# Optimization experiments

Hardware: AMD Instinct MI355X
Metric: run time of the kernel (lower is better)

Reference implementation:

```python
import jax, jax.numpy as jnp
import numpy as np

B, S, D, H, DFF = 2, 4096, 512, 8, 2048
DK = D // H
EPS = 1e-6


def layer_norm(x, alpha, bias):
    # torch: (x - mean) / (std + eps), std unbiased (ddof=1), eps added to std
    mean = jnp.mean(x, axis=-1, keepdims=True)
    std = jnp.std(x, axis=-1, keepdims=True, ddof=1)
    return alpha * (x - mean) / (std + EPS) + bias


def setup_inputs() -> dict:
    key = jax.random.key(0)
    ks = jax.random.split(key, 10)
    s = 0.02
    return {
        "x": jax.random.normal(ks[0], (B, S, D), jnp.float32),
        "mask": jax.random.randint(ks[1], (S, S), 0, 2, jnp.int32),
        "w_q": jax.random.normal(ks[2], (D, D), jnp.float32) * s,
        "w_k": jax.random.normal(ks[3], (D, D), jnp.float32) * s,
        "w_v": jax.random.normal(ks[4], (D, D), jnp.float32) * s,
        "w_o": jax.random.normal(ks[5], (D, D), jnp.float32) * s,
        "w1": jax.random.normal(ks[6], (D, DFF), jnp.float32) * s,
        "b1": jnp.zeros((DFF,), jnp.float32),
        "w2": jax.random.normal(ks[7], (DFF, D), jnp.float32) * s,
        "b2": jnp.zeros((D,), jnp.float32),
        "ln1_a": jnp.ones((D,), jnp.float32),
        "ln1_b": jnp.zeros((D,), jnp.float32),
        "ln2_a": jnp.ones((D,), jnp.float32),
        "ln2_b": jnp.zeros((D,), jnp.float32),
    }


def reference(x, mask, w_q, w_k, w_v, w_o, w1, b1, w2, b2, ln1_a, ln1_b, ln2_a, ln2_b):
    # --- sublayer 0: pre-norm self-attention with residual (dropout=0/eval) ---
    h = layer_norm(x, ln1_a, ln1_b)                       # [B,S,D]
    q = (h @ w_q).reshape(B, S, H, DK)
    k = (h @ w_k).reshape(B, S, H, DK)
    v = (h @ w_v).reshape(B, S, H, DK)
    scores = jnp.einsum("bqhd,bkhd->bhqk", q, k) / jnp.sqrt(jnp.float32(DK))
    scores = jnp.where(mask[None, None, :, :] == 0, jnp.float32(-1e9), scores)
    attn = jax.nn.softmax(scores, axis=-1)                # [B,H,S,S]
    ctx = jnp.einsum("bhqk,bkhd->bqhd", attn, v).reshape(B, S, D)
    x = x + ctx @ w_o
    # --- sublayer 1: pre-norm FFN with residual ---
    h2 = layer_norm(x, ln2_a, ln2_b)
    ff = jax.nn.relu(h2 @ w1 + b1) @ w2 + b2
    return x + ff
```

## Files before the change

### kernel.cpp

```cpp
#include <hip/hip_runtime.h>
#include <hip/hip_bf16.h>
#include <stdint.h>

#define S_LEN 4096
#define DMODEL 512
#define NHEAD 8
#define DHEAD 64
#define NTOK 8192

typedef unsigned short ushort_t;
typedef __attribute__((ext_vector_type(8))) short short8;
typedef __attribute__((ext_vector_type(4))) float f32x4;
typedef unsigned long long u64;
typedef __attribute__((ext_vector_type(2))) unsigned uint2v;

__device__ __forceinline__ float bf2f(ushort_t h) {
    union { unsigned u; float f; } c; c.u = ((unsigned)h) << 16; return c.f;
}
__device__ __forceinline__ ushort_t f2bf(float f) {
    union { float f; unsigned u; } c; c.f = f;
    unsigned u = c.u + 0x7fffu + ((c.u >> 16) & 1u);
    return (ushort_t)(u >> 16);
}
__device__ __forceinline__ void glds16(const ushort_t* g, ushort_t* l) {
    __builtin_amdgcn_global_load_lds(
        (const __attribute__((address_space(1))) unsigned int*)g,
        (__attribute__((address_space(3))) unsigned int*)l, 16, 0, 0);
}

__global__ __launch_bounds__(256) void maskbits_kernel(const int* __restrict__ mask,
        u64* __restrict__ mb) {
    size_t id = (size_t)blockIdx.x * 256 + threadIdx.x;
    int v = mask[id];
    u64 bits = __ballot(v != 0);
    if ((threadIdx.x & 63) == 0) mb[id >> 6] = bits;
}

__global__ __launch_bounds__(256) void masktrans_kernel(const u64* __restrict__ mb,
        u64* __restrict__ mbT) {
    int wid = (int)(((size_t)blockIdx.x * 256 + threadIdx.x) >> 6);
    int lane = threadIdx.x & 63;
    int gq = wid >> 7, kt = wid & 127;
    int lr = lane & 15, lg = lane >> 4;
    int row = gq * 16 + lr;
    u64* outp = mbT + ((size_t)gq * 128 + kt) * 8;
#pragma unroll
    for (int t = 0; t < 2; t++)
#pragma unroll
        for (int r = 0; r < 4; r++) {
            int col = kt * 32 + t * 16 + lg * 4 + r;
            u64 w = mb[(size_t)row * 64 + (col >> 6)];
            u64 bb = __ballot((unsigned)((w >> (col & 63)) & 1));
            if (lane == t * 4 + r) outp[t * 4 + r] = bb;
        }
}

__global__ __launch_bounds__(256) void wtrans_all(const float* __restrict__ wq,
        const float* __restrict__ wk, const float* __restrict__ wv,
        const float* __restrict__ wo, const float* __restrict__ w1,
        const float* __restrict__ w2,
        ushort_t* wqT, ushort_t* wkT, ushort_t* wvT, ushort_t* woT,
        ushort_t* w1T, ushort_t* w2T) {
    __shared__ __attribute__((aligned(16))) ushort_t t[64][72];
    int z = blockIdx.z;
    const float* src; ushort_t* dst; int R, C;
    switch (z) {
        case 0: src = wq; dst = wqT; R = 512;  C = 512;  break;
        case 1: src = wk; dst = wkT; R = 512;  C = 512;  break;
        case 2: src = wv; dst = wvT; R = 512;  C = 512;  break;
        case 3: src = wo; dst = woT; R = 512;  C = 512;  break;
        case 4: src = w1; dst = w1T; R = 512;  C = 2048; break;
        default: src = w2; dst = w2T; R = 2048; C = 512; break;
    }
    int r0 = blockIdx.x * 64, c0 = blockIdx.y * 64;
    if (r0 >= R || c0 >= C) return;
    int tid = threadIdx.x;
    for (int i = tid; i < 4096; i += 256) {
        int r = i >> 6, c = i & 63;
        t[r][c] = f2bf(src[(size_t)(r0 + r) * C + c0 + c]);
    }
    __syncthreads();
    for (int i = tid; i < 512; i += 256) {
        int c = i >> 3, rb = i & 7;
        short8 vv;
#pragma unroll
        for (int j = 0; j < 8; j++) ((ushort_t*)&vv)[j] = t[rb * 8 + j][c];
        *(short8*)(dst + (size_t)(c0 + c) * R + r0 + rb * 8) = vv;
    }
}

__global__ __launch_bounds__(256) void ln_f32(const float* __restrict__ x,
        const float* __restrict__ ga, const float* __restrict__ be,
        ushort_t* __restrict__ out) {
    int tok = blockIdx.x * 4 + (threadIdx.x >> 6);
    int lane = threadIdx.x & 63;
    const float* xr = x + (size_t)tok * DMODEL + lane * 8;
    f32x4 v0 = *(const f32x4*)xr;
    f32x4 v1 = *(const f32x4*)(xr + 4);
    float f[8];
    float s = 0.f, s2 = 0.f;
#pragma unroll
    for (int i = 0; i < 8; i++) {
        f[i] = (i < 4) ? v0[i] : v1[i - 4];
        s += f[i]; s2 += f[i] * f[i];
    }
#pragma unroll
    for (int off = 1; off < 64; off <<= 1) {
        s += __shfl_xor(s, off);
        s2 += __shfl_xor(s2, off);
    }
    float mean = s * (1.f / DMODEL);
    float var = (s2 - (float)DMODEL * mean * mean) * (1.f / (DMODEL - 1));
    var = fmaxf(var, 0.f);
    float inv = 1.f / (sqrtf(var) + 1e-6f);
    short8 o;
#pragma unroll
    for (int i = 0; i < 8; i++) {
        float val = ga[lane * 8 + i] * (f[i] - mean) * inv + be[lane * 8 + i];
        ((ushort_t*)&o)[i] = f2bf(val);
    }
    *(short8*)(out + (size_t)tok * DMODEL + lane * 8) = o;
}

__global__ __launch_bounds__(256) void out_init(const float* __restrict__ x2f,
        const float* __restrict__ b2, float* __restrict__ out) {
    size_t i = ((size_t)blockIdx.x * 256 + threadIdx.x) * 4;
    f32x4 v = *(const f32x4*)(x2f + i);
    f32x4 bb = *(const f32x4*)(b2 + (int)(i & 511));
    v = v + bb;
    *(f32x4*)(out + i) = v;
}

__global__ __launch_bounds__(256) void vtrans(const ushort_t* __restrict__ V,
        ushort_t* __restrict__ VT) {
    __shared__ __attribute__((aligned(16))) ushort_t t[64][72];
    int s0 = blockIdx.x * 64;
    int bh = blockIdx.y;
    int b = bh >> 3, h = bh & 7;
    int tid = threadIdx.x;
    const ushort_t* src = V + ((size_t)b * S_LEN + s0) * DMODEL + h * DHEAD;
    for (int i = tid; i < 512; i += 256) {
        int r = i >> 3, cb = i & 7;
        *(short8*)&t[r][cb * 8] = *(const short8*)(src + (size_t)r * DMODEL + cb * 8);
    }
    __syncthreads();
    ushort_t* dst = VT + (size_t)bh * DHEAD * S_LEN;
    for (int i = tid; i < 512; i += 256) {
        int d = i >> 3, rb = i & 7;
        short8 vv;
#pragma unroll
        for (int j = 0; j < 8; j++) ((ushort_t*)&vv)[j] = t[rb * 8 + j][d];
        *(short8*)(dst + (size_t)d * S_LEN + s0 + rb * 8) = vv;
    }
}

template <int MW, int NW>
__device__ __forceinline__ void gemm_body(const ushort_t* __restrict__ A,
        const ushort_t* __restrict__ BT, void* __restrict__ C,
        int N, int Klen, int kstride, int kbeg, float scale,
        const float* __restrict__ bias, const float* __restrict__ res,
        int relu, int cf32, int atomicc,
        ushort_t* As, ushort_t* Bs, int m0, int n0, int aoff, int coff) {
    int tid = threadIdx.x;
    int wave = tid >> 6, lane = tid & 63;
    int wm = wave >> 1, wn = wave & 1;
    int lr = lane & 15, lg = lane >> 4;
    int srow = lane >> 3, spos = lane & 7;
    int kst = (spos ^ srow) * 8;
    int rdk = lr & 7;
    f32x4 acc[MW][NW];
#pragma unroll
    for (int i = 0; i < MW; i++)
#pragma unroll
        for (int j = 0; j < NW; j++) acc[i][j] = (f32x4){0.f, 0.f, 0.f, 0.f};

    const ushort_t* Ag = A + (size_t)(m0 - aoff) * kstride + kbeg;
    const ushort_t* Bg = BT + (size_t)n0 * kstride + kbeg;

    for (int k0 = 0; k0 < Klen; k0 += 64) {
        __syncthreads();
        for (int ia = wave; ia < 4 * MW; ia += 4)
            glds16(Ag + (size_t)(ia * 8 + srow) * kstride + k0 + kst, As + ia * 8 * 64);
        for (int ib = wave; ib < 4 * NW; ib += 4)
            glds16(Bg + (size_t)(ib * 8 + srow) * kstride + k0 + kst, Bs + ib * 8 * 64);
        __syncthreads();
        short8 af[MW][2], bfv[NW][2];
#pragma unroll
        for (int t = 0; t < MW; t++) {
            const ushort_t* ar = As + (size_t)(wm * 16 * MW + t * 16 + lr) * 64;
            af[t][0] = *(const short8*)(ar + ((lg ^ rdk) * 8));
            af[t][1] = *(const short8*)(ar + (((lg + 4) ^ rdk) * 8));
        }
#pragma unroll
        for (int t = 0; t < NW; t++) {
            const ushort_t* br = Bs + (size_t)(wn * 16 * NW + t * 16 + lr) * 64;
            bfv[t][0] = *(const short8*)(br + ((lg ^ rdk) * 8));
            bfv[t][1] = *(const short8*)(br + (((lg + 4) ^ rdk) * 8));
        }
#pragma unroll
        for (int i = 0; i < MW; i++)
#pragma unroll
            for (int j = 0; j < NW; j++) {
                acc[i][j] = __builtin_amdgcn_mfma_f32_16x16x32_bf16(af[i][0], bfv[j][0], acc[i][j], 0, 0, 0);
                acc[i][j] = __builtin_amdgcn_mfma_f32_16x16x32_bf16(af[i][1], bfv[j][1], acc[i][j], 0, 0, 0);
            }
    }
#pragma unroll
    for (int i = 0; i < MW; i++) {
        int row = m0 + wm * 16 * MW + i * 16 + lg * 4;
#pragma unroll
        for (int j = 0; j < NW; j++) {
            int col = n0 + wn * 16 * NW + j * 16 + lr;
            float bb = bias ? bias[col] : 0.f;
#pragma unroll
            for (int r = 0; r < 4; r++) {
                float v = acc[i][j][r] * scale + bb;
                if (relu) v = fmaxf(v, 0.f);
                if (res) v += res[(size_t)(row + r) * N + col];
                size_t cidx = (size_t)(row + r - coff) * N + col;
                if (atomicc)   atomicAdd((float*)C + cidx, v);
                else if (cf32) ((float*)C)[cidx] = v;
                else           ((ushort_t*)C)[cidx] = f2bf(v);
            }
        }
    }
}

__global__ __launch_bounds__(256) void gemm_bt64(const ushort_t* __restrict__ A,
        const ushort_t* __restrict__ BT, void* __restrict__ C,
        int N, int K, float scale, const float* bias, const float* res, int relu,
        int cf32, int m_base, int aoff, int coff) {
    __shared__ __attribute__((aligned(16))) ushort_t As[64 * 64];
    __shared__ __attribute__((aligned(16))) ushort_t Bs[64 * 64];
    gemm_body<2, 2>(A, BT, C, N, K, K, 0, scale, bias, res, relu, cf32, 0, As, Bs,
                    m_base + blockIdx.x * 64, blockIdx.y * 64, aoff, coff);
}

__global__ __launch_bounds__(256) void gemm_w2sk(const ushort_t* __restrict__ A,
        const ushort_t* __restrict__ BT, float* __restrict__ C,
        int m_base, int aoff) {
    __shared__ __attribute__((aligned(16))) ushort_t As[64 * 64];
    __shared__ __attribute__((aligned(16))) ushort_t Bs[64 * 64];
    int kbeg = blockIdx.z * 1024;
    gemm_body<2, 2>(A, BT, C, 512, 1024, 2048, kbeg, 1.f, nullptr, nullptr, 0, 1, 1,
                    As, Bs, m_base + blockIdx.x * 64, blockIdx.y * 64, aoff, 0);
}

__global__ __launch_bounds__(256) void gemm_qkv(const ushort_t* __restrict__ A,
        const ushort_t* __restrict__ wqT, const ushort_t* __restrict__ wkT,
        const ushort_t* __restrict__ wvT,
        ushort_t* __restrict__ Q, ushort_t* __restrict__ Kb, ushort_t* __restrict__ V) {
    __shared__ __attribute__((aligned(16))) ushort_t As[128 * 64];
    __shared__ __attribute__((aligned(16))) ushort_t Bs[128 * 64];
    int z = blockIdx.z;
    const ushort_t* W = (z == 0) ? wqT : ((z == 1) ? wkT : wvT);
    ushort_t* O = (z == 0) ? Q : ((z == 1) ? Kb : V);
    float sc = (z == 0) ? 0.18033688011112042f : 1.f;
    gemm_body<4, 4>(A, W, O, DMODEL, DMODEL, DMODEL, 0, sc, nullptr, nullptr, 0, 0, 0,
                    As, Bs, blockIdx.x * 128, blockIdx.y * 128, 0, 0);
}

__global__ __launch_bounds__(128, 4) void attn_kernel(const ushort_t* __restrict__ Q,
        const ushort_t* __restrict__ K, const ushort_t* __restrict__ VT,
        const u64* __restrict__ mbT, ushort_t* __restrict__ Opart,
        float* __restrict__ lpart) {
    __shared__ __attribute__((aligned(16))) ushort_t Ks[2][32 * 64];
    __shared__ __attribute__((aligned(16))) ushort_t Vs[2][64 * 32];
    int qt = blockIdx.x, h = blockIdx.y, zz = blockIdx.z;
    int b = zz >> 1, half = zz & 1;
    int tid = threadIdx.x;
    int wv = __builtin_amdgcn_readfirstlane(tid >> 6);
    int lane = tid & 63;
    int lr = lane & 15, lg = lane >> 4;
    size_t tokbase = (size_t)b * S_LEN;
    int q0 = qt * 64 + wv * 32;
    int k0 = half * (S_LEN / 2);

    const ushort_t* Qp = Q + (tokbase + q0) * DMODEL + h * DHEAD;
    short8 qf[2][2];
#pragma unroll
    for (int u = 0; u < 2; u++) {
        qf[u][0] = *(const short8*)(Qp + (size_t)(u * 16 + lr) * DMODEL + lg * 8);
        qf[u][1] = *(const short8*)(Qp + (size_t)(u * 16 + lr) * DMODEL + 32 + lg * 8);
    }
    f32x4 o[2][4];
#pragma unroll
    for (int u = 0; u < 2; u++)
#pragma unroll
        for (int td = 0; td < 4; td++) o[u][td] = (f32x4){0.f, 0.f, 0.f, 0.f};
    f32x4 den[2] = {(f32x4){0.f, 0.f, 0.f, 0.f}, (f32x4){0.f, 0.f, 0.f, 0.f}};
    short8 ones8;
#pragma unroll
    for (int j = 0; j < 8; j++) ((ushort_t*)&ones8)[j] = 0x3F80;

    int srow = lane >> 3, spos = lane & 7;
    int srow2 = lane >> 2, spos2 = lane & 3;
    int kst = (spos ^ srow) * 8;
    int vst = (spos2 ^ ((srow2 >> 1) & 3)) * 8;
    int rdk = lr & 7;
    int rdv = (lr >> 1) & 3;

    const ushort_t* kgl = K + (tokbase + k0) * DMODEL + h * DHEAD
                          + (size_t)srow * DMODEL + kst;
    const ushort_t* vgl = VT + (size_t)(b * NHEAD + h) * DHEAD * S_LEN
                          + (size_t)srow2 * S_LEN + k0 + vst;
    const u64* mq0 = mbT + (((size_t)(q0 >> 4)) * 128 + half * 64) * 8;
    const u64* mq1 = mq0 + 128 * 8;

    if (wv == 0) {
        glds16(kgl + (size_t)0 * DMODEL, &Ks[0][0 * 64]);
        glds16(kgl + (size_t)8 * DMODEL, &Ks[0][8 * 64]);
        glds16(vgl + (size_t)0 * S_LEN, &Vs[0][0 * 32]);
        glds16(vgl + (size_t)16 * S_LEN, &Vs[0][16 * 32]);
    } else {
        glds16(kgl + (size_t)16 * DMODEL, &Ks[0][16 * 64]);
        glds16(kgl + (size_t)24 * DMODEL, &Ks[0][24 * 64]);
        glds16(vgl + (size_t)32 * S_LEN, &Vs[0][32 * 32]);
        glds16(vgl + (size_t)48 * S_LEN, &Vs[0][48 * 32]);
    }

    const int NIT = (S_LEN / 2) / 32;
#pragma unroll 1
    for (int kt = 0; kt < NIT; kt++) {
        int cur = kt & 1;
        const u64* m0 = mq0 + (size_t)kt * 8;
        const u64* m1 = mq1 + (size_t)kt * 8;
        __builtin_amdgcn_s_barrier();
        if (kt + 1 < NIT) {
            const ushort_t* kgn = kgl + (size_t)(kt + 1) * 32 * DMODEL;
            const ushort_t* vgn = vgl + (kt + 1) * 32;
            if (wv == 0) {
                glds16(kgn + (size_t)0 * DMODEL, &Ks[cur ^ 1][0 * 64]);
                glds16(kgn + (size_t)8 * DMODEL, &Ks[cur ^ 1][8 * 64]);
                glds16(vgn + (size_t)0 * S_LEN, &Vs[cur ^ 1][0 * 32]);
                glds16(vgn + (size_t)16 * S_LEN, &Vs[cur ^ 1][16 * 32]);
            } else {
                glds16(kgn + (size_t)16 * DMODEL, &Ks[cur ^ 1][16 * 64]);
                glds16(kgn + (size_t)24 * DMODEL, &Ks[cur ^ 1][24 * 64]);
                glds16(vgn + (size_t)32 * S_LEN, &Vs[cur ^ 1][32 * 32]);
                glds16(vgn + (size_t)48 * S_LEN, &Vs[cur ^ 1][48 * 32]);
            }
            __builtin_amdgcn_s_waitcnt(3956);
        } else {
            __builtin_amdgcn_s_waitcnt(3952);
        }
        __builtin_amdgcn_s_barrier();
        const ushort_t* Kb_ = Ks[cur];
        const ushort_t* Vb_ = Vs[cur];
        f32x4 s[2][2];
#pragma unroll
        for (int t = 0; t < 2; t++) {
            const ushort_t* kr = Kb_ + (t * 16 + lr) * 64;
            short8 kf0 = *(const short8*)(kr + ((lg ^ rdk) * 8));
            short8 kf1 = *(const short8*)(kr + (((lg + 4) ^ rdk) * 8));
#pragma unroll
            for (int u = 0; u < 2; u++) {
                f32x4 z = (f32x4){0.f, 0.f, 0.f, 0.f};
                z = __builtin_amdgcn_mfma_f32_16x16x32_bf16(kf0, qf[u][0], z, 0, 0, 0);
                z = __builtin_amdgcn_mfma_f32_16x16x32_bf16(kf1, qf[u][1], z, 0, 0, 0);
                s[t][u] = z;
            }
        }
#pragma unroll
        for (int u = 0; u < 2; u++) {
            const u64* mu = u ? m1 : m0;
#pragma unroll
            for (int r = 0; r < 4; r++) {
                float p0, p1;
                asm("v_exp_f32 %0, %1\n\ts_nop 0" : "=v"(p0) : "v"(s[0][u][r]));
                asm("v_exp_f32 %0, %1\n\ts_nop 0" : "=v"(p1) : "v"(s[1][u][r]));
                asm("v_cndmask_b32 %0, 0, %1, %2" : "=v"(p0) : "v"(p0), "s"(mu[r]));
                asm("v_cndmask_b32 %0, 0, %1, %2" : "=v"(p1) : "v"(p1), "s"(mu[4 + r]));
                s[0][u][r] = p0; s[1][u][r] = p1;
            }
        }
        short8 vf[4];
#pragma unroll
        for (int td = 0; td < 4; td++)
            vf[td] = *(const short8*)(Vb_ + (td * 16 + lr) * 32 + ((lg ^ rdv) * 8));
#pragma unroll
        for (int u = 0; u < 2; u++) {
            unsigned c00, c01, c10, c11;
            asm("v_cvt_pk_bf16_f32 %0, %1, %2" : "=v"(c00) : "v"(s[0][u][0]), "v"(s[0][u][1]));
            asm("v_cvt_pk_bf16_f32 %0, %1, %2" : "=v"(c01) : "v"(s[0][u][2]), "v"(s[0][u][3]));
            asm("v_cvt_pk_bf16_f32 %0, %1, %2" : "=v"(c10) : "v"(s[1][u][0]), "v"(s[1][u][1]));
            asm("v_cvt_pk_bf16_f32 %0, %1, %2" : "=v"(c11) : "v"(s[1][u][2]), "v"(s[1][u][3]));
            auto r0 = __builtin_amdgcn_permlane32_swap(c00, c10, false, false);
            auto r1 = __builtin_amdgcn_permlane32_swap(c01, c11, false, false);
            auto p0 = __builtin_amdgcn_permlane16_swap(r0[0], r0[1], false, false);
            auto p1 = __builtin_amdgcn_permlane16_swap(r1[0], r1[1], false, false);
            union { unsigned u32[4]; short8 s8; } pk;
            pk.u32[0] = p0[0]; pk.u32[1] = p1[0]; pk.u32[2] = p0[1]; pk.u32[3] = p1[1];
            short8 pf = pk.s8;
#pragma unroll
            for (int td = 0; td < 4; td++)
                o[u][td] = __builtin_amdgcn_mfma_f32_16x16x32_bf16(pf, vf[td], o[u][td], 0, 0, 0);
            den[u] = __builtin_amdgcn_mfma_f32_16x16x32_bf16(pf, ones8, den[u], 0, 0, 0);
        }
    }
    float* lp = lpart + (size_t)half * (NHEAD * 2 * S_LEN)
                + (size_t)(b * NHEAD + h) * S_LEN + q0;
    if (lr == 0) {
#pragma unroll
        for (int u = 0; u < 2; u++)
#pragma unroll
            for (int r = 0; r < 4; r++)
                lp[u * 16 + lg * 4 + r] = den[u][r];
    }
    ushort_t* Op = Opart + (size_t)half * NTOK * DMODEL;
#pragma unroll
    for (int u = 0; u < 2; u++) {
        size_t rowb = (tokbase + q0 + u * 16 + lg * 4) * DMODEL + h * DHEAD;
#pragma unroll
        for (int td = 0; td < 4; td++) {
            int cc = td * 16 + lr;
            Op[rowb + 0 * DMODEL + cc] = f2bf(o[u][td][0]);
            Op[rowb + 1 * DMODEL + cc] = f2bf(o[u][td][1]);
            Op[rowb + 2 * DMODEL + cc] = f2bf(o[u][td][2]);
            Op[rowb + 3 * DMODEL + cc] = f2bf(o[u][td][3]);
        }
    }
}

__global__ __launch_bounds__(256) void attn_combine(const ushort_t* __restrict__ Oa,
        const ushort_t* __restrict__ Ob, const float* __restrict__ la,
        const float* __restrict__ lb, ushort_t* __restrict__ ctx) {
    size_t idx = ((size_t)blockIdx.x * 256 + threadIdx.x) * 8;
    size_t tok = idx >> 9;
    int col = (int)(idx & 511);
    int h = col >> 6;
    int b = (int)(tok >> 12);
    int q = (int)(tok & 4095);
    size_t li = (size_t)(b * NHEAD + h) * S_LEN + q;
    float inv = 1.f / (la[li] + lb[li]);
    short8 va = *(const short8*)(Oa + idx);
    short8 vb = *(const short8*)(Ob + idx);
    short8 oo;
#pragma unroll
    for (int j = 0; j < 8; j++)
        ((ushort_t*)&oo)[j] = f2bf((bf2f(((const ushort_t*)&va)[j])
                                  + bf2f(((const ushort_t*)&vb)[j])) * inv);
    *(short8*)(ctx + idx) = oo;
}

extern "C" void kernel_launch(void* const* d_in, const int* in_sizes, int n_in,
                              void* d_out, int out_size, void* d_ws, size_t ws_size,
                              hipStream_t stream) {
    (void)in_sizes; (void)n_in; (void)out_size; (void)ws_size;
    const float* x    = (const float*)d_in[0];
    const int*   mask = (const int*)d_in[1];
    const float* w_q  = (const float*)d_in[2];
    const float* w_k  = (const float*)d_in[3];
    const float* w_v  = (const float*)d_in[4];
    const float* w_o  = (const float*)d_in[5];
    const float* w1   = (const float*)d_in[6];
    const float* b1   = (const float*)d_in[7];
    const float* w2   = (const float*)d_in[8];
    const float* b2   = (const float*)d_in[9];
    const float* l1a  = (const float*)d_in[10];
    const float* l1b  = (const float*)d_in[11];
    const float* l2a  = (const float*)d_in[12];
    const float* l2b  = (const float*)d_in[13];

    char* ws = (char*)d_ws;
    const size_t MB = 1024 * 1024;
    const size_t KB = 1024;
    ushort_t* w1T  = (ushort_t*)(ws + 0);
    ushort_t* w2T  = (ushort_t*)(ws + 2 * MB);
    ushort_t* wqT  = (ushort_t*)(ws + 4 * MB);
    ushort_t* wkT  = (ushort_t*)(ws + 4 * MB + 512 * KB);
    ushort_t* wvT  = (ushort_t*)(ws + 5 * MB);
    ushort_t* woT  = (ushort_t*)(ws + 5 * MB + 512 * KB);
    ushort_t* ff1  = (ushort_t*)(ws + 6 * MB);
    ushort_t* h    = (ushort_t*)(ws + 22 * MB);
    ushort_t* VTb  = h;
    ushort_t* h2   = h;
    ushort_t* Qb   = (ushort_t*)(ws + 30 * MB);
    float*    x2f  = (float*)(ws + 30 * MB);
    ushort_t* Kb   = (ushort_t*)(ws + 38 * MB);
    ushort_t* Vb   = (ushort_t*)(ws + 46 * MB);
    ushort_t* ctx  = Vb;
    ushort_t* Opart = ff1;
    float*    lpart = (float*)wqT;
    u64*      mb   = (u64*)d_out;
    u64*      mbT  = (u64*)((char*)d_out + 2 * MB);
    float*    out  = (float*)d_out;

    dim3 blk(256);
    maskbits_kernel<<<dim3(65536), blk, 0, stream>>>(mask, mb);
    masktrans_kernel<<<dim3(8192), blk, 0, stream>>>(mb, mbT);
    wtrans_all<<<dim3(32, 32, 6), blk, 0, stream>>>(w_q, w_k, w_v, w_o, w1, w2,
            wqT, wkT, wvT, woT, w1T, w2T);
    ln_f32<<<dim3(NTOK / 4), blk, 0, stream>>>(x, l1a, l1b, h);
    gemm_qkv<<<dim3(64, 4, 3), blk, 0, stream>>>(h, wqT, wkT, wvT, Qb, Kb, Vb);
    vtrans<<<dim3(64, 16), blk, 0, stream>>>(Vb, VTb);
    attn_kernel<<<dim3(64, 8, 4), dim3(128), 0, stream>>>(Qb, Kb, VTb,
            mbT, Opart, lpart);
    attn_combine<<<dim3(2048), blk, 0, stream>>>(Opart,
            Opart + (size_t)NTOK * DMODEL, lpart, lpart + NHEAD * 2 * S_LEN, ctx);
    gemm_bt64<<<dim3(128, 8), blk, 0, stream>>>(ctx, woT, x2f, 512, 512, 1.f,
            nullptr, x, 0, 1, 0, 0, 0);
    ln_f32<<<dim3(NTOK / 4), blk, 0, stream>>>(x2f, l2a, l2b, h2);
    out_init<<<dim3(4096), blk, 0, stream>>>(x2f, b2, out);
    gemm_bt64<<<dim3(64, 32), blk, 0, stream>>>(h2, w1T, ff1, 2048, 512, 1.f,
            b1, nullptr, 1, 0, 0, 0, 0);
    gemm_w2sk<<<dim3(64, 8, 2), blk, 0, stream>>>(ff1, w2T, out, 0, 0);
    gemm_bt64<<<dim3(64, 32), blk, 0, stream>>>(h2, w1T, ff1, 2048, 512, 1.f,
            b1, nullptr, 1, 0, 4096, 0, 4096);
    gemm_w2sk<<<dim3(64, 8, 2), blk, 0, stream>>>(ff1, w2T, out, 4096, 4096);
}
```

Baseline: 405.8 us.

## Fuse mask prep, V transpose, LN2+out init, and double-buffer GEMM tiles

Merges the two mask kernels into one that ballots directly from the int mask, writes V transposed straight from the QKV GEMM epilogue so the separate vtrans kernel goes away, and fuses LayerNorm2 with the residual+bias output init. It also adds a double-buffered LDS variant of the 64x64 GEMM, used for the Wo projection and the split-K W2 GEMM, so the next K tile loads while the current one computes. The goal is fewer launches, fewer intermediate round trips through memory, and hidden global load latency, at the cost of doubled shared memory in those GEMMs and scattered 8-byte stores in the V epilogue.

```diff
diff --git a/kernel.cpp b/kernel.cpp
--- a/kernel.cpp
+++ b/kernel.cpp
@@ -28,31 +28,26 @@
         (__attribute__((address_space(3))) unsigned int*)l, 16, 0, 0);
 }
 
-__global__ __launch_bounds__(256) void maskbits_kernel(const int* __restrict__ mask,
-        u64* __restrict__ mb) {
-    size_t id = (size_t)blockIdx.x * 256 + threadIdx.x;
-    int v = mask[id];
-    u64 bits = __ballot(v != 0);
-    if ((threadIdx.x & 63) == 0) mb[id >> 6] = bits;
-}
-
-__global__ __launch_bounds__(256) void masktrans_kernel(const u64* __restrict__ mb,
+__global__ __launch_bounds__(256) void mask_prep(const int* __restrict__ mask,
         u64* __restrict__ mbT) {
-    int wid = (int)(((size_t)blockIdx.x * 256 + threadIdx.x) >> 6);
-    int lane = threadIdx.x & 63;
-    int gq = wid >> 7, kt = wid & 127;
+    int gq = blockIdx.x;
+    int ktg = blockIdx.y;
+    int wv = threadIdx.x >> 6, lane = threadIdx.x & 63;
     int lr = lane & 15, lg = lane >> 4;
-    int row = gq * 16 + lr;
-    u64* outp = mbT + ((size_t)gq * 128 + kt) * 8;
-#pragma unroll
-    for (int t = 0; t < 2; t++)
-#pragma unroll
-        for (int r = 0; r < 4; r++) {
-            int col = kt * 32 + t * 16 + lg * 4 + r;
-            u64 w = mb[(size_t)row * 64 + (col >> 6)];
-            u64 bb = __ballot((unsigned)((w >> (col & 63)) & 1));
-            if (lane == t * 4 + r) outp[t * 4 + r] = bb;
-        }
+    const int* rowp = mask + (size_t)(gq * 16 + lr) * 4096;
+#pragma unroll
+    for (int j = 0; j < 4; j++) {
+        int kt = ktg * 16 + wv * 4 + j;
+        u64* outp = mbT + ((size_t)gq * 128 + kt) * 8;
+#pragma unroll
+        for (int t = 0; t < 2; t++)
+#pragma unroll
+            for (int r = 0; r < 4; r++) {
+                int v = rowp[kt * 32 + t * 16 + lg * 4 + r];
+                u64 bb = __ballot(v != 0);
+                if (lane == t * 4 + r) outp[t * 4 + r] = bb;
+            }
+    }
 }
 
 __global__ __launch_bounds__(256) void wtrans_all(const float* __restrict__ wq,
@@ -122,40 +117,138 @@
     *(short8*)(out + (size_t)tok * DMODEL + lane * 8) = o;
 }
 
-__global__ __launch_bounds__(256) void out_init(const float* __restrict__ x2f,
-        const float* __restrict__ b2, float* __restrict__ out) {
-    size_t i = ((size_t)blockIdx.x * 256 + threadIdx.x) * 4;
-    f32x4 v = *(const f32x4*)(x2f + i);
-    f32x4 bb = *(const f32x4*)(b2 + (int)(i & 511));
-    v = v + bb;
-    *(f32x4*)(out + i) = v;
-}
-
-__global__ __launch_bounds__(256) void vtrans(const ushort_t* __restrict__ V,
-        ushort_t* __restrict__ VT) {
-    __shared__ __attribute__((aligned(16))) ushort_t t[64][72];
-    int s0 = blockIdx.x * 64;
-    int bh = blockIdx.y;
-    int b = bh >> 3, h = bh & 7;
-    int tid = threadIdx.x;
-    const ushort_t* src = V + ((size_t)b * S_LEN + s0) * DMODEL + h * DHEAD;
-    for (int i = tid; i < 512; i += 256) {
-        int r = i >> 3, cb = i & 7;
-        *(short8*)&t[r][cb * 8] = *(const short8*)(src + (size_t)r * DMODEL + cb * 8);
-    }
-    __syncthreads();
-    ushort_t* dst = VT + (size_t)bh * DHEAD * S_LEN;
-    for (int i = tid; i < 512; i += 256) {
-        int d = i >> 3, rb = i & 7;
-        short8 vv;
-#pragma unroll
-        for (int j = 0; j < 8; j++) ((ushort_t*)&vv)[j] = t[rb * 8 + j][d];
-        *(short8*)(dst + (size_t)d * S_LEN + s0 + rb * 8) = vv;
-    }
+__global__ __launch_bounds__(256) void ln2_out(const float* __restrict__ x2f,
+        const float* __restrict__ ga, const float* __restrict__ be,
+        const float* __restrict__ b2, ushort_t* __restrict__ h2,
+        float* __restrict__ out) {
+    int tok = blockIdx.x * 4 + (threadIdx.x >> 6);
+    int lane = threadIdx.x & 63;
+    const float* xr = x2f + (size_t)tok * DMODEL + lane * 8;
+    f32x4 v0 = *(const f32x4*)xr;
+    f32x4 v1 = *(const f32x4*)(xr + 4);
+    float f[8];
+    float s = 0.f, s2 = 0.f;
+#pragma unroll
+    for (int i = 0; i < 8; i++) {
+        f[i] = (i < 4) ? v0[i] : v1[i - 4];
+        s += f[i]; s2 += f[i] * f[i];
+    }
+#pragma unroll
+    for (int off = 1; off < 64; off <<= 1) {
+        s += __shfl_xor(s, off);
+        s2 += __shfl_xor(s2, off);
+    }
+    float mean = s * (1.f / DMODEL);
+    float var = (s2 - (float)DMODEL * mean * mean) * (1.f / (DMODEL - 1));
+    var = fmaxf(var, 0.f);
+    float inv = 1.f / (sqrtf(var) + 1e-6f);
+    short8 o;
+    f32x4 ob0, ob1;
+#pragma unroll
+    for (int i = 0; i < 8; i++) {
+        float val = ga[lane * 8 + i] * (f[i] - mean) * inv + be[lane * 8 + i];
+        ((ushort_t*)&o)[i] = f2bf(val);
+        float ov = f[i] + b2[lane * 8 + i];
+        if (i < 4) ob0[i] = ov; else ob1[i - 4] = ov;
+    }
+    *(short8*)(h2 + (size_t)tok * DMODEL + lane * 8) = o;
+    float* op = out + (size_t)tok * DMODEL + lane * 8;
+    *(f32x4*)op = ob0;
+    *(f32x4*)(op + 4) = ob1;
 }
 
 template <int MW, int NW>
 __device__ __forceinline__ void gemm_body(const ushort_t* __restrict__ A,
+        const ushort_t* __restrict__ BT, void* __restrict__ C,
+        int N, int Klen, int kstride, int kbeg, float scale,
+        const float* __restrict__ bias, const float* __restrict__ res,
+        int relu, int cf32, int atomicc, int vtw,
+        ushort_t* As, ushort_t* Bs, int m0, int n0, int aoff, int coff) {
+    int tid = threadIdx.x;
+    int wave = tid >> 6, lane = tid & 63;
+    int wm = wave >> 1, wn = wave & 1;
+    int lr = lane & 15, lg = lane >> 4;
+    int srow = lane >> 3, spos = lane & 7;
+    int kst = (spos ^ srow) * 8;
+    int rdk = lr & 7;
+    f32x4 acc[MW][NW];
+#pragma unroll
+    for (int i = 0; i < MW; i++)
+#pragma unroll
+        for (int j = 0; j < NW; j++) acc[i][j] = (f32x4){0.f, 0.f, 0.f, 0.f};
+
+    const ushort_t* Ag = A + (size_t)(m0 - aoff) * kstride + kbeg;
+    const ushort_t* Bg = BT + (size_t)n0 * kstride + kbeg;
+
+    for (int k0 = 0; k0 < Klen; k0 += 64) {
+        __syncthreads();
+        for (int ia = wave; ia < 4 * MW; ia += 4)
+            glds16(Ag + (size_t)(ia * 8 + srow) * kstride + k0 + kst, As + ia * 8 * 64);
+        for (int ib = wave; ib < 4 * NW; ib += 4)
+            glds16(Bg + (size_t)(ib * 8 + srow) * kstride + k0 + kst, Bs + ib * 8 * 64);
+        __syncthreads();
+        short8 af[MW][2], bfv[NW][2];
+#pragma unroll
+        for (int t = 0; t < MW; t++) {
+            const ushort_t* ar = As + (size_t)(wm * 16 * MW + t * 16 + lr) * 64;
+            af[t][0] = *(const short8*)(ar + ((lg ^ rdk) * 8));
+            af[t][1] = *(const short8*)(ar + (((lg + 4) ^ rdk) * 8));
+        }
+#pragma unroll
+        for (int t = 0; t < NW; t++) {
+            const ushort_t* br = Bs + (size_t)(wn * 16 * NW + t * 16 + lr) * 64;
+            bfv[t][0] = *(const short8*)(br + ((lg ^ rdk) * 8));
+            bfv[t][1] = *(const short8*)(br + (((lg + 4) ^ rdk) * 8));
+        }
+#pragma unroll
+        for (int i = 0; i < MW; i++)
+#pragma unroll
+            for (int j = 0; j < NW; j++) {
+                acc[i][j] = __builtin_amdgcn_mfma_f32_16x16x32_bf16(af[i][0], bfv[j][0], acc[i][j], 0, 0, 0);
+                acc[i][j] = __builtin_amdgcn_mfma_f32_16x16x32_bf16(af[i][1], bfv[j][1], acc[i][j], 0, 0, 0);
+            }
+    }
+    if (vtw) {
+#pragma unroll
+        for (int i = 0; i < MW; i++) {
+            int row = m0 + wm * 16 * MW + i * 16 + lg * 4;
+            int bI = row >> 12, sI = row & 4095;
+#pragma unroll
+            for (int j = 0; j < NW; j++) {
+                int col = n0 + wn * 16 * NW + j * 16 + lr;
+                u64 pk = 0;
+#pragma unroll
+                for (int r = 0; r < 4; r++)
+                    pk |= (u64)f2bf(acc[i][j][r] * scale) << (16 * r);
+                *(u64*)((ushort_t*)C
+                    + ((size_t)((bI * 8 + (col >> 6)) * 64 + (col & 63))) * 4096 + sI) = pk;
+            }
+        }
+        return;
+    }
+#pragma unroll
+    for (int i = 0; i < MW; i++) {
+        int row = m0 + wm * 16 * MW + i * 16 + lg * 4;
+#pragma unroll
+        for (int j = 0; j < NW; j++) {
+            int col = n0 + wn * 16 * NW + j * 16 + lr;
+            float bb = bias ? bias[col] : 0.f;
+#pragma unroll
+            for (int r = 0; r < 4; r++) {
+                float v = acc[i][j][r] * scale + bb;
+                if (relu) v = fmaxf(v, 0.f);
+                if (res) v += res[(size_t)(row + r) * N + col];
+                size_t cidx = (size_t)(row + r - coff) * N + col;
+                if (atomicc)   atomicAdd((float*)C + cidx, v);
+                else if (cf32) ((float*)C)[cidx] = v;
+                else           ((ushort_t*)C)[cidx] = f2bf(v);
+            }
+        }
+    }
+}
+
+template <int MW, int NW>
+__device__ __forceinline__ void gemm_body_db(const ushort_t* __restrict__ A,
         const ushort_t* __restrict__ BT, void* __restrict__ C,
         int N, int Klen, int kstride, int kbeg, float scale,
         const float* __restrict__ bias, const float* __restrict__ res,
@@ -176,26 +269,45 @@
 
     const ushort_t* Ag = A + (size_t)(m0 - aoff) * kstride + kbeg;
     const ushort_t* Bg = BT + (size_t)n0 * kstride + kbeg;
-
-    for (int k0 = 0; k0 < Klen; k0 += 64) {
-        __syncthreads();
-        for (int ia = wave; ia < 4 * MW; ia += 4)
-            glds16(Ag + (size_t)(ia * 8 + srow) * kstride + k0 + kst, As + ia * 8 * 64);
-        for (int ib = wave; ib < 4 * NW; ib += 4)
-            glds16(Bg + (size_t)(ib * 8 + srow) * kstride + k0 + kst, Bs + ib * 8 * 64);
-        __syncthreads();
+    const int ASZ = MW * 2048, BSZ = NW * 2048;
+
+    for (int ia = wave; ia < 4 * MW; ia += 4)
+        glds16(Ag + (size_t)(ia * 8 + srow) * kstride + kst, As + ia * 8 * 64);
+    for (int ib = wave; ib < 4 * NW; ib += 4)
+        glds16(Bg + (size_t)(ib * 8 + srow) * kstride + kst, Bs + ib * 8 * 64);
+
+    const int NT = Klen / 64;
+#pragma unroll 1
+    for (int t = 0; t < NT; t++) {
+        int cur = t & 1;
+        __builtin_amdgcn_s_barrier();
+        if (t + 1 < NT) {
+            int k0 = (t + 1) * 64;
+            for (int ia = wave; ia < 4 * MW; ia += 4)
+                glds16(Ag + (size_t)(ia * 8 + srow) * kstride + k0 + kst,
+                       As + (cur ^ 1) * ASZ + ia * 8 * 64);
+            for (int ib = wave; ib < 4 * NW; ib += 4)
+                glds16(Bg + (size_t)(ib * 8 + srow) * kstride + k0 + kst,
+                       Bs + (cur ^ 1) * BSZ + ib * 8 * 64);
+            __builtin_amdgcn_s_waitcnt(3952 + MW + NW);
+        } else {
+            __builtin_amdgcn_s_waitcnt(3952);
+        }
+        __builtin_amdgcn_s_barrier();
+        const ushort_t* Ab = As + cur * ASZ;
+        const ushort_t* Bb = Bs + cur * BSZ;
         short8 af[MW][2], bfv[NW][2];
 #pragma unroll
-        for (int t = 0; t < MW; t++) {
-            const ushort_t* ar = As + (size_t)(wm * 16 * MW + t * 16 + lr) * 64;
-            af[t][0] = *(const short8*)(ar + ((lg ^ rdk) * 8));
-            af[t][1] = *(const short8*)(ar + (((lg + 4) ^ rdk) * 8));
-        }
-#pragma unroll
-        for (int t = 0; t < NW; t++) {
-            const ushort_t* br = Bs + (size_t)(wn * 16 * NW + t * 16 + lr) * 64;
-            bfv[t][0] = *(const short8*)(br + ((lg ^ rdk) * 8));
-            bfv[t][1] = *(const short8*)(br + (((lg + 4) ^ rdk) * 8));
+        for (int q = 0; q < MW; q++) {
+            const ushort_t* ar = Ab + (size_t)(wm * 16 * MW + q * 16 + lr) * 64;
+            af[q][0] = *(const short8*)(ar + ((lg ^ rdk) * 8));
+            af[q][1] = *(const short8*)(ar + (((lg + 4) ^ rdk) * 8));
+        }
+#pragma unroll
+        for (int q = 0; q < NW; q++) {
+            const ushort_t* br = Bb + (size_t)(wn * 16 * NW + q * 16 + lr) * 64;
+            bfv[q][0] = *(const short8*)(br + ((lg ^ rdk) * 8));
+            bfv[q][1] = *(const short8*)(br + (((lg + 4) ^ rdk) * 8));
         }
 #pragma unroll
         for (int i = 0; i < MW; i++)
@@ -232,32 +344,42 @@
         int cf32, int m_base, int aoff, int coff) {
     __shared__ __attribute__((aligned(16))) ushort_t As[64 * 64];
     __shared__ __attribute__((aligned(16))) ushort_t Bs[64 * 64];
-    gemm_body<2, 2>(A, BT, C, N, K, K, 0, scale, bias, res, relu, cf32, 0, As, Bs,
+    gemm_body<2, 2>(A, BT, C, N, K, K, 0, scale, bias, res, relu, cf32, 0, 0, As, Bs,
                     m_base + blockIdx.x * 64, blockIdx.y * 64, aoff, coff);
+}
+
+__global__ __launch_bounds__(256) void gemm_bt64_db(const ushort_t* __restrict__ A,
+        const ushort_t* __restrict__ BT, void* __restrict__ C,
+        int N, int K, float scale, const float* bias, const float* res, int relu,
+        int cf32, int m_base, int aoff, int coff) {
+    __shared__ __attribute__((aligned(16))) ushort_t As[2 * 64 * 64];
+    __shared__ __attribute__((aligned(16))) ushort_t Bs[2 * 64 * 64];
+    gemm_body_db<2, 2>(A, BT, C, N, K, K, 0, scale, bias, res, relu, cf32, 0, As, Bs,
+                       m_base + blockIdx.x * 64, blockIdx.y * 64, aoff, coff);
 }
 
 __global__ __launch_bounds__(256) void gemm_w2sk(const ushort_t* __restrict__ A,
         const ushort_t* __restrict__ BT, float* __restrict__ C,
         int m_base, int aoff) {
-    __shared__ __attribute__((aligned(16))) ushort_t As[64 * 64];
-    __shared__ __attribute__((aligned(16))) ushort_t Bs[64 * 64];
+    __shared__ __attribute__((aligned(16))) ushort_t As[2 * 64 * 64];
+    __shared__ __attribute__((aligned(16))) ushort_t Bs[2 * 64 * 64];
     int kbeg = blockIdx.z * 1024;
-    gemm_body<2, 2>(A, BT, C, 512, 1024, 2048, kbeg, 1.f, nullptr, nullptr, 0, 1, 1,
-                    As, Bs, m_base + blockIdx.x * 64, blockIdx.y * 64, aoff, 0);
+    gemm_body_db<2, 2>(A, BT, C, 512, 1024, 2048, kbeg, 1.f, nullptr, nullptr, 0, 1, 1,
+                       As, Bs, m_base + blockIdx.x * 64, blockIdx.y * 64, aoff, 0);
 }
 
 __global__ __launch_bounds__(256) void gemm_qkv(const ushort_t* __restrict__ A,
         const ushort_t* __restrict__ wqT, const ushort_t* __restrict__ wkT,
         const ushort_t* __restrict__ wvT,
-        ushort_t* __restrict__ Q, ushort_t* __restrict__ Kb, ushort_t* __restrict__ V) {
+        ushort_t* __restrict__ Q, ushort_t* __restrict__ Kb, ushort_t* __restrict__ VT) {
     __shared__ __attribute__((aligned(16))) ushort_t As[128 * 64];
     __shared__ __attribute__((aligned(16))) ushort_t Bs[128 * 64];
     int z = blockIdx.z;
     const ushort_t* W = (z == 0) ? wqT : ((z == 1) ? wkT : wvT);
-    ushort_t* O = (z == 0) ? Q : ((z == 1) ? Kb : V);
+    ushort_t* O = (z == 0) ? Q : ((z == 1) ? Kb : VT);
     float sc = (z == 0) ? 0.18033688011112042f : 1.f;
     gemm_body<4, 4>(A, W, O, DMODEL, DMODEL, DMODEL, 0, sc, nullptr, nullptr, 0, 0, 0,
-                    As, Bs, blockIdx.x * 128, blockIdx.y * 128, 0, 0);
+                    (z == 2) ? 1 : 0, As, Bs, blockIdx.x * 128, blockIdx.y * 128, 0, 0);
 }
 
 __global__ __launch_bounds__(128, 4) void attn_kernel(const ushort_t* __restrict__ Q,
@@ -471,37 +593,32 @@
     ushort_t* wkT  = (ushort_t*)(ws + 4 * MB + 512 * KB);
     ushort_t* wvT  = (ushort_t*)(ws + 5 * MB);
     ushort_t* woT  = (ushort_t*)(ws + 5 * MB + 512 * KB);
+    float*    lpart = (float*)(ws + 4 * MB);
+    ushort_t* Opart = (ushort_t*)(ws + 6 * MB);
     ushort_t* ff1  = (ushort_t*)(ws + 6 * MB);
     ushort_t* h    = (ushort_t*)(ws + 22 * MB);
-    ushort_t* VTb  = h;
-    ushort_t* h2   = h;
+    ushort_t* ctx  = (ushort_t*)(ws + 22 * MB);
+    ushort_t* h2   = (ushort_t*)(ws + 22 * MB);
     ushort_t* Qb   = (ushort_t*)(ws + 30 * MB);
     float*    x2f  = (float*)(ws + 30 * MB);
     ushort_t* Kb   = (ushort_t*)(ws + 38 * MB);
-    ushort_t* Vb   = (ushort_t*)(ws + 46 * MB);
-    ushort_t* ctx  = Vb;
-    ushort_t* Opart = ff1;
-    float*    lpart = (float*)wqT;
-    u64*      mb   = (u64*)d_out;
-    u64*      mbT  = (u64*)((char*)d_out + 2 * MB);
+    ushort_t* VTb  = (ushort_t*)(ws + 46 * MB);
+    u64*      mbT  = (u64*)d_out;
     float*    out  = (float*)d_out;
 
     dim3 blk(256);
-    maskbits_kernel<<<dim3(65536), blk, 0, stream>>>(mask, mb);
-    masktrans_kernel<<<dim3(8192), blk, 0, stream>>>(mb, mbT);
+    mask_prep<<<dim3(256, 8), blk, 0, stream>>>(mask, mbT);
     wtrans_all<<<dim3(32, 32, 6), blk, 0, stream>>>(w_q, w_k, w_v, w_o, w1, w2,
             wqT, wkT, wvT, woT, w1T, w2T);
     ln_f32<<<dim3(NTOK / 4), blk, 0, stream>>>(x, l1a, l1b, h);
-    gemm_qkv<<<dim3(64, 4, 3), blk, 0, stream>>>(h, wqT, wkT, wvT, Qb, Kb, Vb);
-    vtrans<<<dim3(64, 16), blk, 0, stream>>>(Vb, VTb);
+    gemm_qkv<<<dim3(64, 4, 3), blk, 0, stream>>>(h, wqT, wkT, wvT, Qb, Kb, VTb);
     attn_kernel<<<dim3(64, 8, 4), dim3(128), 0, stream>>>(Qb, Kb, VTb,
             mbT, Opart, lpart);
     attn_combine<<<dim3(2048), blk, 0, stream>>>(Opart,
             Opart + (size_t)NTOK * DMODEL, lpart, lpart + NHEAD * 2 * S_LEN, ctx);
-    gemm_bt64<<<dim3(128, 8), blk, 0, stream>>>(ctx, woT, x2f, 512, 512, 1.f,
+    gemm_bt64_db<<<dim3(128, 8), blk, 0, stream>>>(ctx, woT, x2f, 512, 512, 1.f,
             nullptr, x, 0, 1, 0, 0, 0);
-    ln_f32<<<dim3(NTOK / 4), blk, 0, stream>>>(x2f, l2a, l2b, h2);
-    out_init<<<dim3(4096), blk, 0, stream>>>(x2f, b2, out);
+    ln2_out<<<dim3(NTOK / 4), blk, 0, stream>>>(x2f, l2a, l2b, b2, h2, out);
     gemm_bt64<<<dim3(64, 32), blk, 0, stream>>>(h2, w1T, ff1, 2048, 512, 1.f,
             b1, nullptr, 1, 0, 0, 0, 0);
     gemm_w2sk<<<dim3(64, 8, 2), blk, 0, stream>>>(ff1, w2T, out, 0, 0);
```

Measured after the change: 396.9 us. 1.02x faster.
